# Kernel optimization log

Measured on AMD Instinct MI355X. Metric: run time of the kernel, lower is better.

The kernel has to match this reference:

```python
import jax, jax.numpy as jnp
import numpy as np

N = 10000      # atoms
E = 320000     # edges (~32 neighbors/atom)
H = 128        # hidden_channels
F = 128        # num_filters
R = 50         # num_rbf
L = 6          # num_layers
MAXZ = 100
CUT = 5.0      # cutoff_upper (cutoff_lower = 0)


def _cosine_cutoff(d):
    # CosineCutoff with lower=0: 0.5*(cos(pi*d/cut)+1) for d < cut, else 0
    return jnp.where(d < CUT, 0.5 * (jnp.cos(jnp.pi * d / CUT) + 1.0), 0.0)


def _xavier(k, shape):
    fan_in, fan_out = shape[-2], shape[-1]
    lim = np.sqrt(6.0 / (fan_in + fan_out)).astype(np.float32)
    return jax.random.uniform(k, shape, jnp.float32, -lim, lim)


def setup_inputs() -> dict:
    key = jax.random.key(0)
    ks = jax.random.split(key, 16)
    start = float(np.exp(-CUT))  # exp(-cutoff_upper + cutoff_lower)
    return {
        "z": jax.random.randint(ks[0], (N,), 0, MAXZ),
        "pos": jax.random.normal(ks[1], (N, 3), jnp.float32) * 3.0,
        "batch": jnp.zeros((N,), jnp.int32),
        "edge_index": jax.random.randint(ks[2], (2, E), 0, N),
        # nn.Embedding for atom types (main + NeighborEmbedding's own table)
        "emb_table": jax.random.normal(ks[3], (MAXZ, H), jnp.float32),
        "nbr_emb_table": jax.random.normal(ks[4], (MAXZ, H), jnp.float32),
        # NeighborEmbedding: distance_proj (R->H) and combine (2H->H)
        "nbr_proj_W": _xavier(ks[5], (R, H)),
        "nbr_proj_b": jnp.zeros((H,), jnp.float32),
        "nbr_comb_W": _xavier(ks[6], (2 * H, H)),
        "nbr_comb_b": jnp.zeros((H,), jnp.float32),
        # ExpNormalSmearing params (trainable)
        "rbf_means": jnp.linspace(start, 1.0, R, dtype=jnp.float32),
        "rbf_betas": jnp.full((R,), (2.0 / R * (1.0 - start)) ** -2, dtype=jnp.float32),
        # L interaction blocks, params stacked on leading layer dim
        "mlpW1": _xavier(ks[7], (L, R, F)),   # filter net lin1
        "mlpb1": jnp.zeros((L, F), jnp.float32),
        "mlpW2": _xavier(ks[8], (L, F, F)),   # filter net lin2
        "mlpb2": jnp.zeros((L, F), jnp.float32),
        "convW1": _xavier(ks[9], (L, H, F)),  # CFConv lin1 (no bias)
        "convW2": _xavier(ks[10], (L, F, H)), # CFConv lin2
        "convb2": jnp.zeros((L, H), jnp.float32),
        "linW": _xavier(ks[11], (L, H, H)),   # InteractionBlock final lin
        "linb": jnp.zeros((L, H), jnp.float32),
    }


def reference(z, pos, batch, edge_index, emb_table, nbr_emb_table,
              nbr_proj_W, nbr_proj_b, nbr_comb_W, nbr_comb_b,
              rbf_means, rbf_betas, mlpW1, mlpb1, mlpW2, mlpb2,
              convW1, convW2, convb2, linW, linb):
    src, dst = edge_index[0], edge_index[1]
    diff = pos[src] - pos[dst]                       # (E,3)
    d = jnp.sqrt(jnp.sum(diff * diff, axis=-1) + 1e-12)  # edge_weight (E,)
    C = _cosine_cutoff(d)                            # (E,)
    # ExpNormalSmearing: alpha = 5/(cut-0) = 1
    edge_attr = C[:, None] * jnp.exp(
        -rbf_betas * (jnp.exp(-d)[:, None] - rbf_means) ** 2)  # (E,R)

    x = emb_table[z]                                 # (N,H)

    # NeighborEmbedding: self-loops removed, filter modulated by cutoff
    mask = (src != dst).astype(x.dtype)
    Wn = (edge_attr @ nbr_proj_W + nbr_proj_b) * (C * mask)[:, None]  # (E,H)
    msg = jax.ops.segment_sum(nbr_emb_table[z][src] * Wn, dst, num_segments=N)
    x = jnp.concatenate([x, msg], axis=-1) @ nbr_comb_W + nbr_comb_b

    # Interaction blocks: CFConv (gather - filter-MLP - scatter) + residual
    for l in range(L):
        Wf = jax.nn.silu(edge_attr @ mlpW1[l] + mlpb1[l]) @ mlpW2[l] + mlpb2[l]
        Wf = Wf * C[:, None]                         # (E,F)
        y = x @ convW1[l]                            # (N,F), no bias
        m = jax.ops.segment_sum(y[src] * Wf, dst, num_segments=N)  # aggr='add'
        y = jax.nn.silu(m @ convW2[l] + convb2[l])
        y = y @ linW[l] + linb[l]
        x = x + y
    return x
```

## Files before the change

kernel.cpp:

```cpp
#include <hip/hip_runtime.h>
#include <hip/hip_bf16.h>


#define NATOMS 10000
#define NEDGES 320000
#define HC 128
#define RBF 50
#define NLAY 6
#define MAXZ_ 100
#define NK 8192
#define EGRID (NEDGES / 64)
#define YGRID ((NATOMS + 63) / 64)
#define UGRID ((NATOMS + 31) / 32)

typedef __hip_bfloat16 bf16;
typedef __attribute__((ext_vector_type(8))) short bf8v;
typedef __attribute__((ext_vector_type(4))) float f4v;

__device__ __forceinline__ float b2f(bf16 v) { return __bfloat162float(v); }
__device__ __forceinline__ bf16  f2b(float v) { return __float2bfloat16(v); }
__device__ __forceinline__ short f2s(float v) { bf16 h = f2b(v); return *(short*)&h; }
__device__ __forceinline__ float s2f(unsigned short s) {
    return __int_as_float(((int)s) << 16);
}
__device__ __forceinline__ float silu(float v) {
    return v * __builtin_amdgcn_rcpf(1.0f + __expf(-v));
}
__device__ __forceinline__ int isf_of(const int* flagp) {
    return (__int_as_float(flagp[0]) > 1.0e4f) ? 1 : 0;
}

template<int ISF>
__device__ __forceinline__ float LD(const void* p, size_t i) {
    if (ISF) return ((const float*)p)[i];
    return b2f(((const bf16*)p)[i]);
}

__device__ __forceinline__ int clampN(int v) {
    return v < 0 ? 0 : (v >= NATOMS ? NATOMS - 1 : v);
}

template<int ISF>
__device__ __forceinline__ float edge_d(const int* __restrict__ ei,
                                        const void* __restrict__ pos, int e,
                                        int* sOut, int* tOut) {
    int s = clampN(ei[e]);
    int t = clampN(ei[NEDGES + e]);
    *sOut = s; *tOut = t;
    float dx = LD<ISF>(pos, (size_t)s * 3 + 0) - LD<ISF>(pos, (size_t)t * 3 + 0);
    float dy = LD<ISF>(pos, (size_t)s * 3 + 1) - LD<ISF>(pos, (size_t)t * 3 + 1);
    float dz = LD<ISF>(pos, (size_t)s * 3 + 2) - LD<ISF>(pos, (size_t)t * 3 + 2);
    float d = sqrtf(dx * dx + dy * dy + dz * dz + 1e-12f);
    if (d != d) d = 1e30f;
    return d;
}

__global__ void probe_k(const void* pos, int* flag) {
    int i = blockIdx.x * 256 + threadIdx.x;
    float v = 0.0f;
    if (i < NATOMS * 3) {
        v = fabsf(b2f(((const bf16*)pos)[i]));
        if (v != v) v = 1e30f;
    }
    atomicMax(flag, __float_as_int(v));
}

template<int ISF>
__device__ void histd_body(const int* __restrict__ ei, const void* __restrict__ pos,
                           int* __restrict__ counts, float* __restrict__ ed_s,
                           int* __restrict__ src_s, int* __restrict__ dst_s) {
    int e = blockIdx.x * 256 + threadIdx.x;
    if (e >= NEDGES) return;
    ed_s[e] = 0.0f;
    src_s[e] = 0;
    dst_s[e] = NATOMS - 1;
    int s, t;
    float d = edge_d<ISF>(ei, pos, e, &s, &t);
    if (d < 5.0f) atomicAdd(&counts[t], 1);
}
__global__ void histd_k(const int* ei, const void* pos, const int* flagp,
                        int* counts, float* ed_s, int* src_s, int* dst_s) {
    if (isf_of(flagp)) histd_body<1>(ei, pos, counts, ed_s, src_s, dst_s);
    else               histd_body<0>(ei, pos, counts, ed_s, src_s, dst_s);
}

__global__ void scan_k(const int* __restrict__ counts, int* __restrict__ rowptr,
                       int* __restrict__ cursor) {
    __shared__ int wsum[16];
    __shared__ int carry_s;
    __shared__ int chunktot;
    int tid = threadIdx.x, lane = tid & 63, w = tid >> 6;
    if (tid == 0) { carry_s = 0; rowptr[0] = 0; }
    __syncthreads();
    for (int base = 0; base < NATOMS; base += 1024) {
        int i = base + tid;
        int v = (i < NATOMS) ? counts[i] : 0;
        int s = v;
        #pragma unroll
        for (int off = 1; off < 64; off <<= 1) {
            int t = __shfl_up(s, off, 64);
            if (lane >= off) s += t;
        }
        if (lane == 63) wsum[w] = s;
        __syncthreads();
        if (w == 0 && lane < 16) {
            int t = wsum[lane];
            int si = t;
            #pragma unroll
            for (int off = 1; off < 16; off <<= 1) {
                int u = __shfl_up(si, off, 64);
                if (lane >= off) si += u;
            }
            wsum[lane] = si - t;
            if (lane == 15) chunktot = si;
        }
        __syncthreads();
        int carry = carry_s;
        if (i < NATOMS) {
            int inc = carry + wsum[w] + s;
            rowptr[i + 1] = inc;
            cursor[i] = inc - v;
        }
        __syncthreads();
        if (tid == 0) carry_s += chunktot;
        __syncthreads();
    }
}

template<int ISF>
__device__ void permgeom_body(const int* __restrict__ ei, const void* __restrict__ pos,
                              int* __restrict__ cursor,
                              float* __restrict__ ed_s, int* __restrict__ src_s,
                              int* __restrict__ dst_s) {
    int e = blockIdx.x * 256 + threadIdx.x;
    if (e >= NEDGES) return;
    int s, t;
    float d = edge_d<ISF>(ei, pos, e, &s, &t);
    if (d >= 5.0f) return;
    int p = atomicAdd(&cursor[t], 1);
    ed_s[p] = __expf(-d);
    src_s[p] = s;
    dst_s[p] = t;
}
__global__ void permgeom_k(const int* ei, const void* pos, int* cursor, const int* flagp,
                           float* ed_s, int* src_s, int* dst_s) {
    if (isf_of(flagp)) permgeom_body<1>(ei, pos, cursor, ed_s, src_s, dst_s);
    else               permgeom_body<0>(ei, pos, cursor, ed_s, src_s, dst_s);
}

template<int ISF>
__device__ void packB_at(int t, const void* src, int K, int ksteps, size_t perLsrc,
                         size_t perLdst, int L, bf16* dst) {
    if (t >= L * 8 * ksteps * 64) return;
    int lane = t & 63;
    int t2 = t >> 6;
    int ks = t2 % ksteps;
    int t3 = t2 / ksteps;
    int nt = t3 & 7;
    int l  = t3 >> 3;
    int quad = lane >> 4, lc = lane & 15;
    int col = nt * 16 + lc;
    for (int j = 0; j < 8; j++) {
        int k = ks * 32 + quad * 8 + j;
        float v = (k < K) ? LD<ISF>(src, (size_t)l * perLsrc + (size_t)k * 128 + col) : 0.0f;
        dst[(size_t)l * perLdst + ((size_t)((nt * ksteps + ks) * 64 + lane)) * 8 + j] = f2b(v);
    }
}
template<int ISF>
__device__ void packB24_at(int t, const void* w2, const void* cw1, const void* cw2,
                           const void* lw, bf16* w2p, bf16* cw1p, bf16* cw2p, bf16* lwp) {
    if (t >= 24 * 8 * 4 * 64) return;
    int lane = t & 63;
    int t2 = t >> 6;
    int ks = t2 & 3;
    int t3 = t2 >> 2;
    int nt = t3 & 7;
    int m  = t3 >> 3;
    int which = m / NLAY, li = m % NLAY;
    const void* src = which == 0 ? w2 : which == 1 ? cw1 : which == 2 ? cw2 : lw;
    bf16* dst = which == 0 ? w2p : which == 1 ? cw1p : which == 2 ? cw2p : lwp;
    int quad = lane >> 4, lc = lane & 15;
    int col = nt * 16 + lc;
    #pragma unroll
    for (int j = 0; j < 8; j++) {
        int k = ks * 32 + quad * 8 + j;
        float v = LD<ISF>(src, (size_t)li * 16384 + (size_t)k * 128 + col);
        dst[(size_t)li * 16384 + ((size_t)((nt * 4 + ks) * 64 + lane)) * 8 + j] = f2b(v);
    }
}
template<int ISF>
__device__ void cvts_at(int i, const void* means, const void* betas, const void* bp,
                        const void* bc, const void* b1, const void* b2,
                        const void* cb2, const void* lb,
                        float* meanscv, float* betascv, float* bpcv, float* bccv,
                        float* b1cv, float* b2cv, float* cb2cv, float* lbcv) {
    if      (i < 50)   meanscv[i]        = LD<ISF>(means, i);
    else if (i < 100)  betascv[i - 50]   = LD<ISF>(betas, i - 50);
    else if (i < 228)  bpcv[i - 100]     = LD<ISF>(bp, i - 100);
    else if (i < 356)  bccv[i - 228]     = LD<ISF>(bc, i - 228);
    else if (i < 1124) b1cv[i - 356]     = LD<ISF>(b1, i - 356);
    else if (i < 1892) b2cv[i - 1124]    = LD<ISF>(b2, i - 1124);
    else if (i < 2660) cb2cv[i - 1892]   = LD<ISF>(cb2, i - 1892);
    else if (i < 3428) lbcv[i - 2660]    = LD<ISF>(lb, i - 2660);
}
template<int ISF>
__device__ void packall_body(const void* Wp, const void* Wc, const void* W1,
                             const void* W2, const void* cW1, const void* cW2,
                             const void* lW, const void* means, const void* betas,
                             const void* bp, const void* bc, const void* b1,
                             const void* b2, const void* cb2, const void* lb,
                             const void* nbremb,
                             bf16* wpp, bf16* wcp, bf16* w1p, bf16* w2p, bf16* cw1p,
                             bf16* cw2p, bf16* lwp, float* meanscv, float* betascv,
                             float* bpcv, float* bccv, float* b1cv, float* b2cv,
                             float* cb2cv, float* lbcv, bf16* nbrembbf) {
    int b = blockIdx.x, tid = threadIdx.x;
    if (b < 4)        packB_at<ISF>(b * 256 + tid, Wp, RBF, 2, 6400, 8192, 1, wpp);
    else if (b < 20)  packB_at<ISF>((b - 4) * 256 + tid, Wc, 256, 8, 32768, 32768, 1, wcp);
    else if (b < 44)  packB_at<ISF>((b - 20) * 256 + tid, W1, RBF, 2, 6400, 8192, NLAY, w1p);
    else if (b < 236) packB24_at<ISF>((b - 44) * 256 + tid, W2, cW1, cW2, lW,
                                      w2p, cw1p, cw2p, lwp);
    else if (b < 250) cvts_at<ISF>((b - 236) * 256 + tid, means, betas, bp, bc, b1, b2,
                                   cb2, lb, meanscv, betascv, bpcv, bccv,
                                   b1cv, b2cv, cb2cv, lbcv);
    else {
        int i = (b - 250) * 256 + tid;
        if (i < MAXZ_ * HC) nbrembbf[i] = f2b(LD<ISF>(nbremb, i));
    }
}
__global__ void packall_k(const void* Wp, const void* Wc, const void* W1,
                          const void* W2, const void* cW1, const void* cW2,
                          const void* lW, const void* means, const void* betas,
                          const void* bp, const void* bc, const void* b1,
                          const void* b2, const void* cb2, const void* lb,
                          const void* nbremb, const int* flagp,
                          bf16* wpp, bf16* wcp, bf16* w1p, bf16* w2p, bf16* cw1p,
                          bf16* cw2p, bf16* lwp, float* meanscv, float* betascv,
                          float* bpcv, float* bccv, float* b1cv, float* b2cv,
                          float* cb2cv, float* lbcv, bf16* nbrembbf) {
    if (isf_of(flagp)) packall_body<1>(Wp, Wc, W1, W2, cW1, cW2, lW, means, betas,
                                       bp, bc, b1, b2, cb2, lb, nbremb, wpp, wcp,
                                       w1p, w2p, cw1p, cw2p, lwp, meanscv, betascv,
                                       bpcv, bccv, b1cv, b2cv, cb2cv, lbcv, nbrembbf);
    else               packall_body<0>(Wp, Wc, W1, W2, cW1, cW2, lW, means, betas,
                                       bp, bc, b1, b2, cb2, lb, nbremb, wpp, wcp,
                                       w1p, w2p, cw1p, cw2p, lwp, meanscv, betascv,
                                       bpcv, bccv, b1cv, b2cv, cb2cv, lbcv, nbrembbf);
}

#define MFMA(a, b, c) __builtin_amdgcn_mfma_f32_16x16x32_bf16((a), (b), (c), 0, 0, 0)

__device__ __forceinline__ void seg_prep(const int* __restrict__ dst_s, int i0, int tid,
                                         int* ddst, int* slot_s, int* distinct_s,
                                         int* nseg_s) {
    if (tid < 64) {
        int d = dst_s[i0 + tid];
        ddst[tid] = d;
        int dprev = __shfl_up(d, 1, 64);
        int flag = (tid == 0 || d != dprev) ? 1 : 0;
        int s = flag;
        #pragma unroll
        for (int off = 1; off < 64; off <<= 1) {
            int t = __shfl_up(s, off, 64);
            if (tid >= off) s += t;
        }
        slot_s[tid] = s - 1;
        if (flag) distinct_s[s - 1] = d;
        if (tid == 63) *nseg_s = s;
    }
}

__device__ __forceinline__ void seg_mfma(const bf16 (*mvT)[72], const int* ddst,
                                         const int* slot_s, const int* distinct_s,
                                         int nseg, float* __restrict__ out, int tid) {
    int wave = tid >> 6, lane = tid & 63, quad = lane >> 4, lc = lane & 15;
    if (nseg <= 16) {
        bf8v sa[2];
        #pragma unroll
        for (int ks = 0; ks < 2; ks++)
            #pragma unroll
            for (int j = 0; j < 8; j++) {
                int k = ks * 32 + quad * 8 + j;
                sa[ks][j] = (slot_s[k] == lc) ? (short)0x3F80 : (short)0;
            }
        f4v z4 = {0.f, 0.f, 0.f, 0.f};
        f4v sacc[2] = {z4, z4};
        #pragma unroll
        for (int nt = 0; nt < 2; nt++)
            #pragma unroll
            for (int ks = 0; ks < 2; ks++) {
                bf8v b = *(const bf8v*)&mvT[wave * 32 + nt * 16 + lc][ks * 32 + quad * 8];
                sacc[nt] = MFMA(sa[ks], b, sacc[nt]);
            }
        #pragma unroll
        for (int nt = 0; nt < 2; nt++)
            #pragma unroll
            for (int r = 0; r < 4; r++) {
                int sl = quad * 4 + r;
                if (sl < nseg) {
                    int atom = distinct_s[sl];
                    int n = wave * 32 + nt * 16 + lc;
                    float v = sacc[nt][r];
                    if (sl == 0 || sl == nseg - 1)
                        atomicAdd(&out[(size_t)atom * HC + n], v);
                    else
                        out[(size_t)atom * HC + n] = v;
                }
            }
    } else {
        int col = tid & 127;
        int base = (tid >> 7) * 32;
        int cur = ddst[base];
        float s = 0.0f;
        bool first = true;
        for (int e = base; e < base + 32; e++) {
            int dn = ddst[e];
            if (dn != cur) {
                if (first) atomicAdd(&out[(size_t)cur * HC + col], s);
                else out[(size_t)cur * HC + col] = s;
                first = false; cur = dn; s = 0.0f;
            }
            s += b2f(mvT[col][e]);
        }
        atomicAdd(&out[(size_t)cur * HC + col], s);
    }
}

__global__ __launch_bounds__(256)
void tabbuild_k(const bf16* __restrict__ wpp, const float* __restrict__ bpcv,
                const bf16* __restrict__ w1p, const float* __restrict__ b1cv,
                const bf16* __restrict__ w2p, const float* __restrict__ b2cv,
                const float* __restrict__ meanscv, const float* __restrict__ betascv,
                bf16* __restrict__ Tb) {
    __shared__ bf16 hid[64][136];
    __shared__ float csh[64], edsh[64];
    int f = blockIdx.x >> 7, kb = blockIdx.x & 127;
    int base = kb * 64;
    int tid = threadIdx.x;
    int wave = tid >> 6, lane = tid & 63, quad = lane >> 4, lc = lane & 15;
    if (tid < 64) {
        float ed = (float)(base + tid) * (1.0f / (NK - 1));
        float d = -logf(fmaxf(ed, 1e-30f));
        float C = (d < 5.0f) ? 0.5f * (__cosf(d * 0.6283185307f) + 1.0f) : 0.0f;
        csh[tid] = C; edsh[tid] = ed;
    }
    __syncthreads();
    float edi = edsh[wave * 16 + lc], Ci = csh[wave * 16 + lc];
    bf8v af[2];
    #pragma unroll
    for (int ks = 0; ks < 2; ks++) {
        #pragma unroll
        for (int j = 0; j < 8; j++) {
            int r = ks * 32 + quad * 8 + j;
            float v = 0.0f;
            if (r < RBF) { float u = edi - meanscv[r]; v = Ci * __expf(-betascv[r] * u * u); }
            af[ks][j] = f2s(v);
        }
    }
    f4v zero = {0.f, 0.f, 0.f, 0.f};
    f4v acc[8];
    #pragma unroll
    for (int nt = 0; nt < 8; nt++) acc[nt] = zero;
    const bf16* w1b = (f == 0) ? wpp : w1p + (size_t)(f - 1) * 8192;
    #pragma unroll
    for (int nt = 0; nt < 8; nt++)
        #pragma unroll
        for (int ks = 0; ks < 2; ks++) {
            bf8v b = *(const bf8v*)(w1b + ((nt * 2 + ks) * 64 + lane) * 8);
            acc[nt] = MFMA(af[ks], b, acc[nt]);
        }
    if (f == 0) {
        #pragma unroll
        for (int nt = 0; nt < 8; nt++) {
            int n = nt * 16 + lc;
            float bb = bpcv[n];
            #pragma unroll
            for (int r = 0; r < 4; r++) {
                int row = wave * 16 + quad * 4 + r;
                Tb[(size_t)(base + row) * HC + n] = f2b((acc[nt][r] + bb) * csh[row]);
            }
        }
        return;
    }
    int l = f - 1;
    #pragma unroll
    for (int nt = 0; nt < 8; nt++) {
        int n = nt * 16 + lc;
        float bb = b1cv[l * HC + n];
        #pragma unroll
        for (int r = 0; r < 4; r++)
            hid[wave * 16 + quad * 4 + r][n] = f2b(silu(acc[nt][r] + bb));
    }
    __syncthreads();
    bf8v a2[4];
    #pragma unroll
    for (int ks = 0; ks < 4; ks++)
        a2[ks] = *(const bf8v*)&hid[wave * 16 + lc][ks * 32 + quad * 8];
    f4v acc2[8];
    #pragma unroll
    for (int nt = 0; nt < 8; nt++) acc2[nt] = zero;
    const bf16* w2b = w2p + (size_t)l * 16384;
    #pragma unroll
    for (int nt = 0; nt < 8; nt++)
        #pragma unroll
        for (int ks = 0; ks < 4; ks++) {
            bf8v b = *(const bf8v*)(w2b + ((nt * 4 + ks) * 64 + lane) * 8);
            acc2[nt] = MFMA(a2[ks], b, acc2[nt]);
        }
    #pragma unroll
    for (int nt = 0; nt < 8; nt++) {
        int n = nt * 16 + lc;
        float bb = b2cv[l * HC + n];
        #pragma unroll
        for (int r = 0; r < 4; r++) {
            int row = wave * 16 + quad * 4 + r;
            Tb[((size_t)f * NK + base + row) * HC + n] = f2b((acc2[nt][r] + bb) * csh[row]);
        }
    }
}

__global__ __launch_bounds__(256)
void nbr_tab_k(const int* __restrict__ rowptr,
               const float* __restrict__ ed_s, const int* __restrict__ src_s,
               const int* __restrict__ dst_s, const int* __restrict__ z,
               const bf16* __restrict__ nbrembbf, const bf16* __restrict__ Tb,
               float* __restrict__ msg) {
    __shared__ bf16 mvT[128][72];
    __shared__ int ddst[64], slot_s[64], distinct_s[64];
    __shared__ int nseg_s;
    int i0 = blockIdx.x * 64;
    if (i0 >= rowptr[NATOMS]) return;
    int tid = threadIdx.x;
    seg_prep(dst_s, i0, tid, ddst, slot_s, distinct_s, &nseg_s);
    int row = tid & 63, c0 = (tid >> 6) * 32;
    int e = i0 + row;
    int s = src_s[e];
    float msk = (s != dst_s[e]) ? 1.0f : 0.0f;
    float pos = fminf(fmaxf(ed_s[e] * (float)(NK - 1) + 0.5f, 0.0f), (float)(NK - 1));
    int k = (int)pos;
    const bf8v* tp = (const bf8v*)(Tb + (size_t)k * HC + c0);
    bf8v tv[4];
    #pragma unroll
    for (int g = 0; g < 4; g++) tv[g] = tp[g];
    int zz = z[s]; zz = zz < 0 ? 0 : (zz >= MAXZ_ ? MAXZ_ - 1 : zz);
    const bf8v* ep = (const bf8v*)(nbrembbf + (size_t)zz * HC + c0);
    bf8v ev[4];
    #pragma unroll
    for (int g = 0; g < 4; g++) ev[g] = ep[g];
    #pragma unroll
    for (int g = 0; g < 4; g++)
        #pragma unroll
        for (int m = 0; m < 8; m++) {
            float v = s2f((unsigned short)tv[g][m]) * msk *
                      s2f((unsigned short)ev[g][m]);
            mvT[c0 + g * 8 + m][row] = f2b(v);
        }
    __syncthreads();
    seg_mfma(mvT, ddst, slot_s, distinct_s, nseg_s, msg, tid);
}

template<int ISF>
__device__ void combine_body(const int* __restrict__ z, const void* __restrict__ emb,
                             const float* __restrict__ msg, const bf16* __restrict__ wcp,
                             const float* __restrict__ bccv, const bf16* __restrict__ cw1b,
                             float* __restrict__ x, bf16* __restrict__ xb,
                             bf16* __restrict__ ybf) {
    __shared__ bf16 srow[64][136];
    int tid = threadIdx.x;
    int wave = tid >> 6, lane = tid & 63, quad = lane >> 4, lc = lane & 15;
    int m0 = blockIdx.x * 64;
    int arow = m0 + wave * 16 + lc;
    int rowc = arow < NATOMS ? arow : NATOMS - 1;
    int zz = z[rowc]; zz = zz < 0 ? 0 : (zz >= MAXZ_ ? MAXZ_ - 1 : zz);
    bf8v af[8];
    #pragma unroll
    for (int ks = 0; ks < 4; ks++)
        #pragma unroll
        for (int j = 0; j < 8; j++)
            af[ks][j] = f2s(LD<ISF>(emb, (size_t)zz * HC + ks * 32 + quad * 8 + j));
    #pragma unroll
    for (int ks = 4; ks < 8; ks++) {
        const float* mp = msg + (size_t)rowc * HC + (ks - 4) * 32 + quad * 8;
        #pragma unroll
        for (int j = 0; j < 8; j++) af[ks][j] = f2s(mp[j]);
    }
    f4v zero = {0.f, 0.f, 0.f, 0.f};
    f4v acc[8];
    #pragma unroll
    for (int nt = 0; nt < 8; nt++) acc[nt] = zero;
    #pragma unroll
    for (int nt = 0; nt < 8; nt++)
        #pragma unroll
        for (int ks = 0; ks < 8; ks++) {
            bf8v b = *(const bf8v*)(wcp + ((nt * 8 + ks) * 64 + lane) * 8);
            acc[nt] = MFMA(af[ks], b, acc[nt]);
        }
    #pragma unroll
    for (int nt = 0; nt < 8; nt++) {
        int n = nt * 16 + lc;
        float bb = bccv[n];
        #pragma unroll
        for (int r = 0; r < 4; r++) {
            int row = m0 + wave * 16 + quad * 4 + r;
            float v = acc[nt][r] + bb;
            bf16 vb = f2b(v);
            srow[wave * 16 + quad * 4 + r][n] = vb;
            if (row < NATOMS) {
                x[(size_t)row * HC + n] = v;
                xb[(size_t)row * HC + n] = vb;
            }
        }
    }
    __syncthreads();
    bf8v a3[4];
    #pragma unroll
    for (int ks = 0; ks < 4; ks++)
        a3[ks] = *(const bf8v*)&srow[wave * 16 + lc][ks * 32 + quad * 8];
    f4v acc3[8];
    #pragma unroll
    for (int nt = 0; nt < 8; nt++) acc3[nt] = zero;
    #pragma unroll
    for (int nt = 0; nt < 8; nt++)
        #pragma unroll
        for (int ks = 0; ks < 4; ks++) {
            bf8v b = *(const bf8v*)(cw1b + ((nt * 4 + ks) * 64 + lane) * 8);
            acc3[nt] = MFMA(a3[ks], b, acc3[nt]);
        }
    #pragma unroll
    for (int nt = 0; nt < 8; nt++) {
        int n = nt * 16 + lc;
        #pragma unroll
        for (int r = 0; r < 4; r++) {
            int row = m0 + wave * 16 + quad * 4 + r;
            if (row < NATOMS) ybf[(size_t)row * HC + n] = f2b(acc3[nt][r]);
        }
    }
}
__global__ __launch_bounds__(256)
void combine_k(const int* z, const void* emb, const float* msg, const bf16* wcp,
               const float* bccv, const bf16* cw1b, const int* flagp,
               float* x, bf16* xb, bf16* ybf) {
    if (isf_of(flagp)) combine_body<1>(z, emb, msg, wcp, bccv, cw1b, x, xb, ybf);
    else               combine_body<0>(z, emb, msg, wcp, bccv, cw1b, x, xb, ybf);
}

__global__ __launch_bounds__(256)
void filt_tab_k(int l, const int* __restrict__ rowptr,
                const float* __restrict__ ed_s, const int* __restrict__ src_s,
                const int* __restrict__ dst_s, const bf16* __restrict__ ybf,
                const bf16* __restrict__ Tb, float* __restrict__ msum) {
    __shared__ bf16 mvT[128][72];
    __shared__ int ddst[64], slot_s[64], distinct_s[64];
    __shared__ int nseg_s;
    int i0 = blockIdx.x * 64;
    if (i0 >= rowptr[NATOMS]) return;
    int tid = threadIdx.x;
    seg_prep(dst_s, i0, tid, ddst, slot_s, distinct_s, &nseg_s);
    int row = tid & 63, c0 = (tid >> 6) * 32;
    int e = i0 + row;
    float pos = fminf(fmaxf(ed_s[e] * (float)(NK - 1) + 0.5f, 0.0f), (float)(NK - 1));
    int k = (int)pos;
    const bf8v* tp = (const bf8v*)(Tb + ((size_t)(l + 1) * NK + k) * HC + c0);
    bf8v tv[4];
    #pragma unroll
    for (int g = 0; g < 4; g++) tv[g] = tp[g];
    const bf8v* yp = (const bf8v*)(ybf + (size_t)src_s[e] * HC + c0);
    bf8v yv[4];
    #pragma unroll
    for (int g = 0; g < 4; g++) yv[g] = yp[g];
    #pragma unroll
    for (int g = 0; g < 4; g++)
        #pragma unroll
        for (int m = 0; m < 8; m++) {
            float v = s2f((unsigned short)tv[g][m]) * s2f((unsigned short)yv[g][m]);
            mvT[c0 + g * 8 + m][row] = f2b(v);
        }
    __syncthreads();
    seg_mfma(mvT, ddst, slot_s, distinct_s, nseg_s, msum, tid);
}

__global__ __launch_bounds__(256)
void upd_mfma_k(float* msum, int l,
                const bf16* __restrict__ cw2p, const float* __restrict__ cb2cv,
                const bf16* __restrict__ lwp, const float* __restrict__ lbcv,
                const bf16* __restrict__ cw1p, int do_y, int last,
                float* __restrict__ x, bf16* __restrict__ xb,
                bf16* __restrict__ ybf, void* out, const int* flagp) {
    __shared__ bf16 srow[32][136];
    int tid = threadIdx.x;
    int wave = tid >> 6, lane = tid & 63, quad = lane >> 4, lc = lane & 15;
    int rb = wave >> 1, ch = wave & 1;
    int m0 = blockIdx.x * 32 + rb * 16;
    bf8v azero = {0, 0, 0, 0, 0, 0, 0, 0};
    bf8v af[4];
    int arow = m0 + lc;
    #pragma unroll
    for (int ks = 0; ks < 4; ks++) {
        if (arow < NATOMS) {
            const float* p = msum + (size_t)arow * HC + ks * 32 + quad * 8;
            bf8v f;
            #pragma unroll
            for (int j = 0; j < 8; j++) f[j] = f2s(p[j]);
            af[ks] = f;
        } else af[ks] = azero;
    }
    f4v zero = {0.f, 0.f, 0.f, 0.f};
    f4v acc[4];
    #pragma unroll
    for (int nt = 0; nt < 4; nt++) acc[nt] = zero;
    const bf16* c2b = cw2p + (size_t)l * 16384;
    #pragma unroll
    for (int nt = 0; nt < 4; nt++)
        #pragma unroll
        for (int ks = 0; ks < 4; ks++) {
            bf8v b = *(const bf8v*)(c2b + (((ch * 4 + nt) * 4 + ks) * 64 + lane) * 8);
            acc[nt] = MFMA(af[ks], b, acc[nt]);
        }
    #pragma unroll
    for (int nt = 0; nt < 4; nt++) {
        int n = ch * 64 + nt * 16 + lc;
        float bb = cb2cv[l * HC + n];
        #pragma unroll
        for (int r = 0; r < 4; r++)
            srow[rb * 16 + quad * 4 + r][n] = f2b(silu(acc[nt][r] + bb));
    }
    __syncthreads();
    if (ch == 0 && arow < NATOMS) {
        float zdep = fminf(fabsf(acc[0][0]), 0.0f);
        f4v zv = {zdep, zdep, zdep, zdep};
        #pragma unroll
        for (int ks = 0; ks < 4; ks++) {
            *(f4v*)(msum + (size_t)arow * HC + ks * 32 + quad * 8) = zv;
            *(f4v*)(msum + (size_t)arow * HC + ks * 32 + quad * 8 + 4) = zv;
        }
    }
    bf8v a2[4];
    #pragma unroll
    for (int ks = 0; ks < 4; ks++)
        a2[ks] = *(const bf8v*)&srow[rb * 16 + lc][ks * 32 + quad * 8];
    __syncthreads();
    f4v acc2[4];
    #pragma unroll
    for (int nt = 0; nt < 4; nt++) acc2[nt] = zero;
    const bf16* lwb = lwp + (size_t)l * 16384;
    #pragma unroll
    for (int nt = 0; nt < 4; nt++)
        #pragma unroll
        for (int ks = 0; ks < 4; ks++) {
            bf8v b = *(const bf8v*)(lwb + (((ch * 4 + nt) * 4 + ks) * 64 + lane) * 8);
            acc2[nt] = MFMA(a2[ks], b, acc2[nt]);
        }
    int isf = isf_of(flagp);
    #pragma unroll
    for (int nt = 0; nt < 4; nt++) {
        int n = ch * 64 + nt * 16 + lc;
        float bb = lbcv[l * HC + n];
        #pragma unroll
        for (int r = 0; r < 4; r++) {
            int row = m0 + quad * 4 + r;
            float nv = 0.0f;
            if (row < NATOMS) {
                size_t o = (size_t)row * HC + n;
                nv = x[o] + acc2[nt][r] + bb;
                if (!last) {
                    x[o] = nv;
                    xb[o] = f2b(nv);
                } else {
                    if (isf) ((float*)out)[o] = nv;
                    else     ((bf16*)out)[o] = f2b(nv);
                }
            }
            srow[rb * 16 + quad * 4 + r][n] = f2b(nv);
        }
    }
    if (do_y) {
        __syncthreads();
        bf8v a3[4];
        #pragma unroll
        for (int ks = 0; ks < 4; ks++)
            a3[ks] = *(const bf8v*)&srow[rb * 16 + lc][ks * 32 + quad * 8];
        f4v acc3[4];
        #pragma unroll
        for (int nt = 0; nt < 4; nt++) acc3[nt] = zero;
        const bf16* c1b = cw1p + (size_t)(l + 1) * 16384;
        #pragma unroll
        for (int nt = 0; nt < 4; nt++)
            #pragma unroll
            for (int ks = 0; ks < 4; ks++) {
                bf8v b = *(const bf8v*)(c1b + (((ch * 4 + nt) * 4 + ks) * 64 + lane) * 8);
                acc3[nt] = MFMA(a3[ks], b, acc3[nt]);
            }
        #pragma unroll
        for (int nt = 0; nt < 4; nt++) {
            int n = ch * 64 + nt * 16 + lc;
            #pragma unroll
            for (int r = 0; r < 4; r++) {
                int row = m0 + quad * 4 + r;
                if (row < NATOMS) ybf[(size_t)row * HC + n] = f2b(acc3[nt][r]);
            }
        }
    }
}

extern "C" void kernel_launch(void* const* d_in, const int* in_sizes, int n_in,
                              void* d_out, int out_size, void* d_ws, size_t ws_size,
                              hipStream_t stream) {
    const int*  z      = (const int*) d_in[0];
    const void* pos    = d_in[1];
    const int*  ei     = (const int*) d_in[3];
    const void* emb    = d_in[4];
    const void* nbremb = d_in[5];
    const void* Wp     = d_in[6];
    const void* bp     = d_in[7];
    const void* Wc     = d_in[8];
    const void* bc     = d_in[9];
    const void* means  = d_in[10];
    const void* betas  = d_in[11];
    const void* W1     = d_in[12];
    const void* b1     = d_in[13];
    const void* W2     = d_in[14];
    const void* b2     = d_in[15];
    const void* cW1    = d_in[16];
    const void* cW2    = d_in[17];
    const void* cb2    = d_in[18];
    const void* lW     = d_in[19];
    const void* lb     = d_in[20];

    char* p = (char*)d_ws;
    auto alloc = [&](size_t bytes) { char* r = p; p += (bytes + 255) / 256 * 256; return r; };
    int*   flag    = (int*)  alloc(256);
    int*   counts  = (int*)  alloc((size_t)NATOMS * 4);
    float* msum    = (float*)alloc((size_t)NATOMS * HC * 4);
    float* msg     = (float*)alloc((size_t)NATOMS * HC * 4);
    int*   rowptr  = (int*)  alloc((size_t)(NATOMS + 1) * 4);
    int*   cursor  = (int*)  alloc((size_t)NATOMS * 4);
    int*   src_s   = (int*)  alloc((size_t)NEDGES * 4);
    int*   dst_s   = (int*)  alloc((size_t)NEDGES * 4);
    float* ed_s    = (float*)alloc((size_t)NEDGES * 4);
    float* x       = (float*)alloc((size_t)NATOMS * HC * 4);
    bf16*  xb      = (bf16*) alloc((size_t)NATOMS * HC * 2);
    bf16*  ybf     = (bf16*) alloc((size_t)NATOMS * HC * 2);
    bf16*  Tb      = (bf16*) alloc((size_t)(NLAY + 1) * NK * HC * 2);
    bf16*  wpp     = (bf16*) alloc((size_t)8192 * 2);
    bf16*  wcp     = (bf16*) alloc((size_t)32768 * 2);
    bf16*  w1p     = (bf16*) alloc((size_t)NLAY * 8192 * 2);
    bf16*  w2p     = (bf16*) alloc((size_t)NLAY * 16384 * 2);
    bf16*  cw1p    = (bf16*) alloc((size_t)NLAY * 16384 * 2);
    bf16*  cw2p    = (bf16*) alloc((size_t)NLAY * 16384 * 2);
    bf16*  lwp     = (bf16*) alloc((size_t)NLAY * 16384 * 2);
    bf16*  nbrembbf= (bf16*) alloc((size_t)MAXZ_ * HC * 2);
    float* bpcv    = (float*)alloc((size_t)HC * 4);
    float* bccv    = (float*)alloc((size_t)HC * 4);
    float* b1cv    = (float*)alloc((size_t)NLAY * HC * 4);
    float* b2cv    = (float*)alloc((size_t)NLAY * HC * 4);
    float* cb2cv   = (float*)alloc((size_t)NLAY * HC * 4);
    float* lbcv    = (float*)alloc((size_t)NLAY * HC * 4);
    float* meanscv = (float*)alloc((size_t)RBF * 4);
    float* betascv = (float*)alloc((size_t)RBF * 4);

    const int EG = (NEDGES + 255) / 256;

    size_t zbytes = 256 + ((size_t)NATOMS * 4 + 255) / 256 * 256
                  + (size_t)2 * NATOMS * HC * 4;
    hipMemsetAsync(flag, 0, zbytes, stream);
    probe_k<<<(NATOMS * 3 + 255) / 256, 256, 0, stream>>>(pos, flag);
    histd_k<<<EG, 256, 0, stream>>>(ei, pos, flag, counts, ed_s, src_s, dst_s);
    scan_k<<<1, 1024, 0, stream>>>(counts, rowptr, cursor);
    permgeom_k<<<EG, 256, 0, stream>>>(ei, pos, cursor, flag, ed_s, src_s, dst_s);

    packall_k<<<300, 256, 0, stream>>>(Wp, Wc, W1, W2, cW1, cW2, lW, means, betas,
                                       bp, bc, b1, b2, cb2, lb, nbremb, flag,
                                       wpp, wcp, w1p, w2p, cw1p, cw2p, lwp,
                                       meanscv, betascv, bpcv, bccv, b1cv, b2cv,
                                       cb2cv, lbcv, nbrembbf);
    tabbuild_k<<<7 * (NK / 64), 256, 0, stream>>>(wpp, bpcv, w1p, b1cv, w2p, b2cv,
                                                  meanscv, betascv, Tb);

    nbr_tab_k<<<EGRID, 256, 0, stream>>>(rowptr, ed_s, src_s, dst_s, z, nbrembbf, Tb, msg);
    combine_k<<<YGRID, 256, 0, stream>>>(z, emb, msg, wcp, bccv, cw1p, flag, x, xb, ybf);

    for (int l = 0; l < NLAY; l++) {
        filt_tab_k<<<EGRID, 256, 0, stream>>>(l, rowptr, ed_s, src_s, dst_s, ybf, Tb, msum);
        int lastl = (l == NLAY - 1) ? 1 : 0;
        upd_mfma_k<<<UGRID, 256, 0, stream>>>(msum, l, cw2p, cb2cv, lwp, lbcv,
                                              cw1p, lastl ? 0 : 1, lastl,
                                              x, xb, ybf, d_out, flag);
    }
}
```

Measured before the change: 362.6 us.

## Shrink update tile to 16 rows, cache edge distances, single-pass scan

The node-update MFMA kernel now processes 16 rows per block with four waves splitting 128 output columns, which doubles the grid and drops bounds checks because NATOMS divides by 16. The distance computed in the histogram pass is stored and reused in the permutation pass instead of regathering positions. The scan now does a single pass with 10 elements per thread instead of a chunked loop with several barriers, and the probe kernel reduces within a wave before its atomic. The cost is an extra edge-sized buffer write and read, plus more blocks that each reload the weight tiles.

```diff
diff --git a/kernel.cpp b/kernel.cpp
--- a/kernel.cpp
+++ b/kernel.cpp
@@ -11,7 +11,7 @@
 #define NK 8192
 #define EGRID (NEDGES / 64)
 #define YGRID ((NATOMS + 63) / 64)
-#define UGRID ((NATOMS + 31) / 32)
+#define UGRID (NATOMS / 16)
 
 typedef __hip_bfloat16 bf16;
 typedef __attribute__((ext_vector_type(8))) short bf8v;
@@ -62,13 +62,17 @@
         v = fabsf(b2f(((const bf16*)pos)[i]));
         if (v != v) v = 1e30f;
     }
-    atomicMax(flag, __float_as_int(v));
+    #pragma unroll
+    for (int off = 32; off > 0; off >>= 1)
+        v = fmaxf(v, __shfl_xor(v, off, 64));
+    if ((threadIdx.x & 63) == 0) atomicMax(flag, __float_as_int(v));
 }
 
 template<int ISF>
 __device__ void histd_body(const int* __restrict__ ei, const void* __restrict__ pos,
                            int* __restrict__ counts, float* __restrict__ ed_s,
-                           int* __restrict__ src_s, int* __restrict__ dst_s) {
+                           int* __restrict__ src_s, int* __restrict__ dst_s,
+                           float* __restrict__ d_raw) {
     int e = blockIdx.x * 256 + threadIdx.x;
     if (e >= NEDGES) return;
     ed_s[e] = 0.0f;
@@ -76,76 +80,75 @@
     dst_s[e] = NATOMS - 1;
     int s, t;
     float d = edge_d<ISF>(ei, pos, e, &s, &t);
+    d_raw[e] = d;
     if (d < 5.0f) atomicAdd(&counts[t], 1);
 }
 __global__ void histd_k(const int* ei, const void* pos, const int* flagp,
-                        int* counts, float* ed_s, int* src_s, int* dst_s) {
-    if (isf_of(flagp)) histd_body<1>(ei, pos, counts, ed_s, src_s, dst_s);
-    else               histd_body<0>(ei, pos, counts, ed_s, src_s, dst_s);
+                        int* counts, float* ed_s, int* src_s, int* dst_s,
+                        float* d_raw) {
+    if (isf_of(flagp)) histd_body<1>(ei, pos, counts, ed_s, src_s, dst_s, d_raw);
+    else               histd_body<0>(ei, pos, counts, ed_s, src_s, dst_s, d_raw);
 }
 
 __global__ void scan_k(const int* __restrict__ counts, int* __restrict__ rowptr,
                        int* __restrict__ cursor) {
     __shared__ int wsum[16];
-    __shared__ int carry_s;
-    __shared__ int chunktot;
     int tid = threadIdx.x, lane = tid & 63, w = tid >> 6;
-    if (tid == 0) { carry_s = 0; rowptr[0] = 0; }
-    __syncthreads();
-    for (int base = 0; base < NATOMS; base += 1024) {
-        int i = base + tid;
-        int v = (i < NATOMS) ? counts[i] : 0;
-        int s = v;
-        #pragma unroll
-        for (int off = 1; off < 64; off <<= 1) {
-            int t = __shfl_up(s, off, 64);
-            if (lane >= off) s += t;
-        }
-        if (lane == 63) wsum[w] = s;
-        __syncthreads();
-        if (w == 0 && lane < 16) {
-            int t = wsum[lane];
-            int si = t;
-            #pragma unroll
-            for (int off = 1; off < 16; off <<= 1) {
-                int u = __shfl_up(si, off, 64);
-                if (lane >= off) si += u;
-            }
-            wsum[lane] = si - t;
-            if (lane == 15) chunktot = si;
-        }
-        __syncthreads();
-        int carry = carry_s;
+    int base = tid * 10;
+    int v[10];
+    int s = 0;
+    #pragma unroll
+    for (int j = 0; j < 10; j++) {
+        int i = base + j;
+        int c = (i < NATOMS) ? counts[i] : 0;
+        v[j] = c; s += c;
+    }
+    int si = s;
+    #pragma unroll
+    for (int off = 1; off < 64; off <<= 1) {
+        int t = __shfl_up(si, off, 64);
+        if (lane >= off) si += t;
+    }
+    if (lane == 63) wsum[w] = si;
+    __syncthreads();
+    if (w == 0 && lane < 16) {
+        int t = wsum[lane];
+        int s2 = t;
+        #pragma unroll
+        for (int off = 1; off < 16; off <<= 1) {
+            int u = __shfl_up(s2, off, 64);
+            if (lane >= off) s2 += u;
+        }
+        wsum[lane] = s2 - t;
+    }
+    __syncthreads();
+    int run = wsum[w] + si - s;
+    #pragma unroll
+    for (int j = 0; j < 10; j++) {
+        int i = base + j;
         if (i < NATOMS) {
-            int inc = carry + wsum[w] + s;
-            rowptr[i + 1] = inc;
-            cursor[i] = inc - v;
-        }
-        __syncthreads();
-        if (tid == 0) carry_s += chunktot;
-        __syncthreads();
-    }
-}
-
-template<int ISF>
-__device__ void permgeom_body(const int* __restrict__ ei, const void* __restrict__ pos,
-                              int* __restrict__ cursor,
-                              float* __restrict__ ed_s, int* __restrict__ src_s,
-                              int* __restrict__ dst_s) {
+            cursor[i] = run;
+            run += v[j];
+            rowptr[i + 1] = run;
+        }
+    }
+    if (tid == 0) rowptr[0] = 0;
+}
+
+__global__ void permgeom_k(const int* __restrict__ ei, const float* __restrict__ d_raw,
+                           int* __restrict__ cursor,
+                           float* __restrict__ ed_s, int* __restrict__ src_s,
+                           int* __restrict__ dst_s) {
     int e = blockIdx.x * 256 + threadIdx.x;
     if (e >= NEDGES) return;
-    int s, t;
-    float d = edge_d<ISF>(ei, pos, e, &s, &t);
+    float d = d_raw[e];
     if (d >= 5.0f) return;
+    int s = clampN(ei[e]);
+    int t = clampN(ei[NEDGES + e]);
     int p = atomicAdd(&cursor[t], 1);
     ed_s[p] = __expf(-d);
     src_s[p] = s;
     dst_s[p] = t;
-}
-__global__ void permgeom_k(const int* ei, const void* pos, int* cursor, const int* flagp,
-                           float* ed_s, int* src_s, int* dst_s) {
-    if (isf_of(flagp)) permgeom_body<1>(ei, pos, cursor, ed_s, src_s, dst_s);
-    else               permgeom_body<0>(ei, pos, cursor, ed_s, src_s, dst_s);
 }
 
 template<int ISF>
@@ -586,91 +589,75 @@
                 const bf16* __restrict__ cw1p, int do_y, int last,
                 float* __restrict__ x, bf16* __restrict__ xb,
                 bf16* __restrict__ ybf, void* out, const int* flagp) {
-    __shared__ bf16 srow[32][136];
+    __shared__ bf16 srow[16][136];
     int tid = threadIdx.x;
-    int wave = tid >> 6, lane = tid & 63, quad = lane >> 4, lc = lane & 15;
-    int rb = wave >> 1, ch = wave & 1;
-    int m0 = blockIdx.x * 32 + rb * 16;
-    bf8v azero = {0, 0, 0, 0, 0, 0, 0, 0};
+    int w = tid >> 6, lane = tid & 63, quad = lane >> 4, lc = lane & 15;
+    int m0 = blockIdx.x * 16;
     bf8v af[4];
-    int arow = m0 + lc;
     #pragma unroll
     for (int ks = 0; ks < 4; ks++) {
-        if (arow < NATOMS) {
-            const float* p = msum + (size_t)arow * HC + ks * 32 + quad * 8;
-            bf8v f;
-            #pragma unroll
-            for (int j = 0; j < 8; j++) f[j] = f2s(p[j]);
-            af[ks] = f;
-        } else af[ks] = azero;
+        const float* p = msum + (size_t)(m0 + lc) * HC + ks * 32 + quad * 8;
+        bf8v f;
+        #pragma unroll
+        for (int j = 0; j < 8; j++) f[j] = f2s(p[j]);
+        af[ks] = f;
     }
     f4v zero = {0.f, 0.f, 0.f, 0.f};
-    f4v acc[4];
-    #pragma unroll
-    for (int nt = 0; nt < 4; nt++) acc[nt] = zero;
+    f4v acc[2] = {zero, zero};
     const bf16* c2b = cw2p + (size_t)l * 16384;
     #pragma unroll
-    for (int nt = 0; nt < 4; nt++)
+    for (int nt = 0; nt < 2; nt++)
         #pragma unroll
         for (int ks = 0; ks < 4; ks++) {
-            bf8v b = *(const bf8v*)(c2b + (((ch * 4 + nt) * 4 + ks) * 64 + lane) * 8);
+            bf8v b = *(const bf8v*)(c2b + (((w * 2 + nt) * 4 + ks) * 64 + lane) * 8);
             acc[nt] = MFMA(af[ks], b, acc[nt]);
         }
     #pragma unroll
-    for (int nt = 0; nt < 4; nt++) {
-        int n = ch * 64 + nt * 16 + lc;
+    for (int nt = 0; nt < 2; nt++) {
+        int n = w * 32 + nt * 16 + lc;
         float bb = cb2cv[l * HC + n];
         #pragma unroll
         for (int r = 0; r < 4; r++)
-            srow[rb * 16 + quad * 4 + r][n] = f2b(silu(acc[nt][r] + bb));
-    }
-    __syncthreads();
-    if (ch == 0 && arow < NATOMS) {
-        float zdep = fminf(fabsf(acc[0][0]), 0.0f);
-        f4v zv = {zdep, zdep, zdep, zdep};
+            srow[quad * 4 + r][n] = f2b(silu(acc[nt][r] + bb));
+    }
+    __syncthreads();
+    {
+        int zr = tid >> 4, zc = (tid & 15) * 8;
+        *(f4v*)(msum + (size_t)(m0 + zr) * HC + zc) = zero;
+        *(f4v*)(msum + (size_t)(m0 + zr) * HC + zc + 4) = zero;
+    }
+    bf8v a2[4];
+    #pragma unroll
+    for (int ks = 0; ks < 4; ks++)
+        a2[ks] = *(const bf8v*)&srow[lc][ks * 32 + quad * 8];
+    __syncthreads();
+    f4v acc2[2] = {zero, zero};
+    const bf16* lwb = lwp + (size_t)l * 16384;
+    #pragma unroll
+    for (int nt = 0; nt < 2; nt++)
         #pragma unroll
         for (int ks = 0; ks < 4; ks++) {
-            *(f4v*)(msum + (size_t)arow * HC + ks * 32 + quad * 8) = zv;
-            *(f4v*)(msum + (size_t)arow * HC + ks * 32 + quad * 8 + 4) = zv;
-        }
-    }
-    bf8v a2[4];
-    #pragma unroll
-    for (int ks = 0; ks < 4; ks++)
-        a2[ks] = *(const bf8v*)&srow[rb * 16 + lc][ks * 32 + quad * 8];
-    __syncthreads();
-    f4v acc2[4];
-    #pragma unroll
-    for (int nt = 0; nt < 4; nt++) acc2[nt] = zero;
-    const bf16* lwb = lwp + (size_t)l * 16384;
-    #pragma unroll
-    for (int nt = 0; nt < 4; nt++)
-        #pragma unroll
-        for (int ks = 0; ks < 4; ks++) {
-            bf8v b = *(const bf8v*)(lwb + (((ch * 4 + nt) * 4 + ks) * 64 + lane) * 8);
+            bf8v b = *(const bf8v*)(lwb + (((w * 2 + nt) * 4 + ks) * 64 + lane) * 8);
             acc2[nt] = MFMA(a2[ks], b, acc2[nt]);
         }
     int isf = isf_of(flagp);
     #pragma unroll
-    for (int nt = 0; nt < 4; nt++) {
-        int n = ch * 64 + nt * 16 + lc;
+    for (int nt = 0; nt < 2; nt++) {
+        int n = w * 32 + nt * 16 + lc;
         float bb = lbcv[l * HC + n];
         #pragma unroll
         for (int r = 0; r < 4; r++) {
             int row = m0 + quad * 4 + r;
-            float nv = 0.0f;
-            if (row < NATOMS) {
-                size_t o = (size_t)row * HC + n;
-                nv = x[o] + acc2[nt][r] + bb;
-                if (!last) {
-                    x[o] = nv;
-                    xb[o] = f2b(nv);
-                } else {
-                    if (isf) ((float*)out)[o] = nv;
-                    else     ((bf16*)out)[o] = f2b(nv);
-                }
-            }
-            srow[rb * 16 + quad * 4 + r][n] = f2b(nv);
+            size_t o = (size_t)row * HC + n;
+            float nv = x[o] + acc2[nt][r] + bb;
+            if (!last) {
+                x[o] = nv;
+                xb[o] = f2b(nv);
+            } else {
+                if (isf) ((float*)out)[o] = nv;
+                else     ((bf16*)out)[o] = f2b(nv);
+            }
+            srow[quad * 4 + r][n] = f2b(nv);
         }
     }
     if (do_y) {
@@ -678,25 +665,23 @@
         bf8v a3[4];
         #pragma unroll
         for (int ks = 0; ks < 4; ks++)
-            a3[ks] = *(const bf8v*)&srow[rb * 16 + lc][ks * 32 + quad * 8];
-        f4v acc3[4];
-        #pragma unroll
-        for (int nt = 0; nt < 4; nt++) acc3[nt] = zero;
+            a3[ks] = *(const bf8v*)&srow[lc][ks * 32 + quad * 8];
+        f4v acc3[2] = {zero, zero};
         const bf16* c1b = cw1p + (size_t)(l + 1) * 16384;
         #pragma unroll
-        for (int nt = 0; nt < 4; nt++)
+        for (int nt = 0; nt < 2; nt++)
             #pragma unroll
             for (int ks = 0; ks < 4; ks++) {
-                bf8v b = *(const bf8v*)(c1b + (((ch * 4 + nt) * 4 + ks) * 64 + lane) * 8);
+                bf8v b = *(const bf8v*)(c1b + (((w * 2 + nt) * 4 + ks) * 64 + lane) * 8);
                 acc3[nt] = MFMA(a3[ks], b, acc3[nt]);
             }
         #pragma unroll
-        for (int nt = 0; nt < 4; nt++) {
-            int n = ch * 64 + nt * 16 + lc;
+        for (int nt = 0; nt < 2; nt++) {
+            int n = w * 32 + nt * 16 + lc;
             #pragma unroll
             for (int r = 0; r < 4; r++) {
                 int row = m0 + quad * 4 + r;
-                if (row < NATOMS) ybf[(size_t)row * HC + n] = f2b(acc3[nt][r]);
+                ybf[(size_t)row * HC + n] = f2b(acc3[nt][r]);
             }
         }
     }
@@ -737,6 +722,7 @@
     int*   src_s   = (int*)  alloc((size_t)NEDGES * 4);
     int*   dst_s   = (int*)  alloc((size_t)NEDGES * 4);
     float* ed_s    = (float*)alloc((size_t)NEDGES * 4);
+    float* d_raw   = (float*)alloc((size_t)NEDGES * 4);
     float* x       = (float*)alloc((size_t)NATOMS * HC * 4);
     bf16*  xb      = (bf16*) alloc((size_t)NATOMS * HC * 2);
     bf16*  ybf     = (bf16*) alloc((size_t)NATOMS * HC * 2);
@@ -764,9 +750,9 @@
                   + (size_t)2 * NATOMS * HC * 4;
     hipMemsetAsync(flag, 0, zbytes, stream);
     probe_k<<<(NATOMS * 3 + 255) / 256, 256, 0, stream>>>(pos, flag);
-    histd_k<<<EG, 256, 0, stream>>>(ei, pos, flag, counts, ed_s, src_s, dst_s);
+    histd_k<<<EG, 256, 0, stream>>>(ei, pos, flag, counts, ed_s, src_s, dst_s, d_raw);
     scan_k<<<1, 1024, 0, stream>>>(counts, rowptr, cursor);
-    permgeom_k<<<EG, 256, 0, stream>>>(ei, pos, cursor, flag, ed_s, src_s, dst_s);
+    permgeom_k<<<EG, 256, 0, stream>>>(ei, d_raw, cursor, ed_s, src_s, dst_s);
 
     packall_k<<<300, 256, 0, stream>>>(Wp, Wc, W1, W2, cW1, cW2, lW, means, betas,
                                        bp, bc, b1, b2, cb2, lb, nbremb, flag,
```

Measured after the change: 336.6 us. 7.2% less time.
